# Performance work log

Measured on AMD Instinct MI355X. Metric: run time of the kernel, lower is better.

Reference implementation:

```python
import jax, jax.numpy as jnp
import numpy as np

DIM = 1024
HEADS = 16
HEAD_DIM = DIM // HEADS
SCALE = HEAD_DIM ** -0.5


def setup_inputs() -> dict:
    key = jax.random.key(0)
    k_x, k_win, k_wout, k_bout = jax.random.split(key, 4)
    x = jax.random.normal(k_x, (4, 2048, DIM), dtype=jnp.float32)
    # torch Linear: y = x @ W.T + b; store weights as [in, out] for jnp
    w_in = jax.random.normal(k_win, (DIM, 3 * DIM), dtype=jnp.float32) * (DIM ** -0.5)
    w_out = jax.random.normal(k_wout, (DIM, DIM), dtype=jnp.float32) * (DIM ** -0.5)
    b_out = jax.random.normal(k_bout, (DIM,), dtype=jnp.float32) * 0.02
    return {"x": x, "w_in": w_in, "w_out": w_out, "b_out": b_out}


def reference(x, w_in, w_out, b_out):
    b, n, _ = x.shape
    qkv = x @ w_in  # [b, n, 3*dim]
    q, k, v = jnp.split(qkv, 3, axis=-1)
    # [b, n, h*d] -> [b, h, n, d]
    def split_heads(t):
        return t.reshape(b, n, HEADS, HEAD_DIM).transpose(0, 2, 1, 3)
    q, k, v = split_heads(q), split_heads(k), split_heads(v)
    scores = jnp.einsum('bhid,bhjd->bhij', q, k) * SCALE
    attn = jax.nn.softmax(scores, axis=-1)  # dropout_rate=0 -> identity
    o = jnp.einsum('bhij,bhjd->bhid', attn, v)
    o = o.transpose(0, 2, 1, 3).reshape(b, n, HEADS * HEAD_DIM)
    return o @ w_out + b_out
```

## Files before the change

### kernel.cpp

```cpp
#include <hip/hip_runtime.h>

typedef unsigned short u16;
typedef __bf16 bf16x8 __attribute__((ext_vector_type(8)));
typedef float f32x4 __attribute__((ext_vector_type(4)));
typedef unsigned short u16x4 __attribute__((ext_vector_type(4)));
typedef unsigned short u16x8 __attribute__((ext_vector_type(8)));

#define DIM 1024
#define HEADS 16
#define HD 64
#define SEQ 2048
#define BATCH 4
#define NROWS (BATCH*SEQ)
#define C2 0.18033688f
#define THR_PS 1.125899907e15f

__device__ __forceinline__ u16 f2bf(float f) {
  union { float f; unsigned u; } v; v.f = f;
  unsigned r = v.u + 0x7FFFu + ((v.u >> 16) & 1u);
  return (u16)(r >> 16);
}

__device__ __forceinline__ unsigned cvt_pk_bf16(float lo, float hi) {
  unsigned r;
  asm("v_cvt_pk_bf16_f32 %0, %1, %2" : "=v"(r) : "v"(lo), "v"(hi));
  return r;
}

__device__ __forceinline__ f32x4 mfma16(bf16x8 a, bf16x8 b, f32x4 c) {
  return __builtin_amdgcn_mfma_f32_16x16x32_bf16(a, b, c, 0, 0, 0);
}

__device__ __forceinline__ void gl_lds16(const void* g, void* l) {
  __builtin_amdgcn_global_load_lds(
      (const __attribute__((address_space(1))) void*)g,
      (__attribute__((address_space(3))) void*)l, 16, 0, 0);
}

__global__ __launch_bounds__(256) void prep_kernel(const float* __restrict__ x,
                                                   const float* __restrict__ w_in,
                                                   const float* __restrict__ w_out,
                                                   u16* __restrict__ xb,
                                                   u16* __restrict__ w_inT,
                                                   u16* __restrict__ w_outT) {
  __shared__ u16 tile[64][65];
  const int bid = blockIdx.x;
  const int tid = threadIdx.x;
  if (bid < 8192) {
    int i = bid * 256 + tid;
    float4 v = ((const float4*)x)[i];
    u16x4 o = { f2bf(v.x), f2bf(v.y), f2bf(v.z), f2bf(v.w) };
    *(u16x4*)(xb + (size_t)i * 4) = o;
    return;
  }
  const float* in;
  u16* out;
  int R, C, c0, r0;
  if (bid < 8960) {
    int b2 = bid - 8192;
    in = w_in; out = w_inT; R = 1024; C = 3072;
    c0 = (b2 % 48) * 64; r0 = (b2 / 48) * 64;
  } else {
    int b3 = bid - 8960;
    in = w_out; out = w_outT; R = 1024; C = 1024;
    c0 = (b3 % 16) * 64; r0 = (b3 / 16) * 64;
  }
#pragma unroll
  for (int i = 0; i < 16; ++i) {
    int idx = tid + i * 256;
    int r = idx >> 6, c = idx & 63;
    tile[c][r] = f2bf(in[(size_t)(r0 + r) * C + c0 + c]);
  }
  __syncthreads();
#pragma unroll
  for (int i = 0; i < 16; ++i) {
    int idx = tid + i * 256;
    int r = idx >> 6, c = idx & 63;
    out[(size_t)(c0 + r) * R + r0 + c] = tile[r][c];
  }
}

__global__ __launch_bounds__(256) void transpose_v(const u16* __restrict__ qkv,
                                                   u16* __restrict__ vT) {
  __shared__ unsigned t32[64][37];
  const int t = blockIdx.x, bh = blockIdx.y;
  const int b = bh >> 4, h = bh & 15;
  const u16* src = qkv + ((size_t)(b * SEQ + t * 64)) * 3072 + 2048 + h * 64;
  const int tid = threadIdx.x;
#pragma unroll
  for (int i = 0; i < 8; ++i) {
    int lin = tid + i * 256;
    int r2 = lin >> 6, c = lin & 63;
    unsigned lo = src[(size_t)(2 * r2) * 3072 + c];
    unsigned hi = src[(size_t)(2 * r2 + 1) * 3072 + c];
    t32[c][r2] = lo | (hi << 16);
  }
  __syncthreads();
  unsigned* dst = (unsigned*)(vT + (size_t)bh * 64 * 2048);
#pragma unroll
  for (int i = 0; i < 8; ++i) {
    int lin = tid + i * 256;
    int d = lin >> 5, r2 = lin & 31;
    int rp = (r2 & 16) | ((r2 & 6) << 1) | ((r2 & 8) >> 2) | (r2 & 1);
    dst[(size_t)d * 1024 + t * 32 + rp] = t32[d][r2];
  }
}

template<int OUT_F32>
__global__ __launch_bounds__(256) void gemm_bt(const u16* __restrict__ A,
                                               const u16* __restrict__ BT,
                                               void* __restrict__ Cout,
                                               const float* __restrict__ bias,
                                               int M, int N, int K, int nx) {
  __shared__ __align__(16) u16 As[128 * 64];
  __shared__ __align__(16) u16 Bs[128 * 64];
  const int tid = threadIdx.x;
  const int l = tid & 63, w = tid >> 6, g = l >> 4, ln = l & 15;
  const int cpx = gridDim.x >> 3;
  const int jj = (blockIdx.x & 7) * cpx + (blockIdx.x >> 3);
  const int n0 = (jj % nx) * 128, m0 = (jj / nx) * 128;
  const int wr = w >> 1, wc = w & 1;
  f32x4 acc[4][4];
#pragma unroll
  for (int i = 0; i < 4; ++i)
#pragma unroll
    for (int j = 0; j < 4; ++j) acc[i][j] = (f32x4){0.f, 0.f, 0.f, 0.f};

  const int srow = tid >> 3;
  const int scol = (tid & 7) * 8;
  const u16* Asrc = A  + (size_t)(m0 + srow) * K + scol;
  const u16* Bsrc = BT + (size_t)(n0 + srow) * K + scol;
  char* AsB = (char*)As + (size_t)w * 1024;
  char* BsB = (char*)Bs + (size_t)w * 1024;

  const int nk = K >> 6;
  for (int kt = 0; kt < nk; ++kt) {
    const u16* a0 = Asrc + kt * 64;
    const u16* b0 = Bsrc + kt * 64;
#pragma unroll
    for (int is = 0; is < 4; ++is) {
      gl_lds16(a0 + (size_t)is * 32 * K, AsB + is * 4096);
      gl_lds16(b0 + (size_t)is * 32 * K, BsB + is * 4096);
    }
    __syncthreads();
#pragma unroll
    for (int kk = 0; kk < 2; ++kk) {
      bf16x8 af[4], bfr[4];
#pragma unroll
      for (int i = 0; i < 4; ++i) {
        af[i]  = *(const bf16x8*)(As + (wr * 64 + i * 16 + ln) * 64 + kk * 32 + g * 8);
        bfr[i] = *(const bf16x8*)(Bs + (wc * 64 + i * 16 + ln) * 64 + kk * 32 + g * 8);
      }
#pragma unroll
      for (int mi = 0; mi < 4; ++mi)
#pragma unroll
        for (int ni = 0; ni < 4; ++ni)
          acc[mi][ni] = mfma16(af[mi], bfr[ni], acc[mi][ni]);
    }
    __syncthreads();
  }
#pragma unroll
  for (int mi = 0; mi < 4; ++mi) {
#pragma unroll
    for (int ni = 0; ni < 4; ++ni) {
      int col = n0 + wc * 64 + ni * 16 + ln;
#pragma unroll
      for (int j = 0; j < 4; ++j) {
        int row = m0 + wr * 64 + mi * 16 + g * 4 + j;
        float v = acc[mi][ni][j];
        if (OUT_F32) {
          ((float*)Cout)[(size_t)row * N + col] = v + bias[col];
        } else {
          ((u16*)Cout)[(size_t)row * N + col] = f2bf(v);
        }
      }
    }
  }
}

__global__ __launch_bounds__(256) void attn_kernel(const u16* __restrict__ qkv,
                                                   const u16* __restrict__ vT,
                                                   u16* __restrict__ obuf) {
  __shared__ __align__(16) u16 k_lds[2][64 * 64];
  __shared__ __align__(16) u16 v_lds[2][64 * 64];
  const int wg = blockIdx.x;
  const int j = (wg & 7) * 128 + (wg >> 3);
  const int qt = j & 15, h = (j >> 4) & 15, b = j >> 8;
  const int tid = threadIdx.x;
  const int w = tid >> 6, l = tid & 63, g = l >> 4, ln = l & 15;
  const int qbase = qt * 128 + w * 32;
  const size_t rs = 3 * DIM;

  bf16x8 qf[2][2];
#pragma unroll
  for (int e = 0; e < 2; ++e) {
    const u16* qb = qkv + (size_t)(b * SEQ + qbase + e * 16 + ln) * rs + h * HD;
    qf[e][0] = *(const bf16x8*)(qb + g * 8);
    qf[e][1] = *(const bf16x8*)(qb + 32 + g * 8);
  }

  const int krow = tid >> 3;
  const int ksrccol = ((((tid & 7) << 4) ^ ((krow & 7) << 4))) >> 1;
  const u16* kbase = qkv + (size_t)b * SEQ * rs + DIM + h * HD;
  const u16* vtb = vT + (size_t)(b * HEADS + h) * 64 * 2048;
  const int swz = (ln & 7) << 4;

  float m[2] = { -1e30f, -1e30f }, psac[2] = { 0.f, 0.f };
  f32x4 of[2][4];
#pragma unroll
  for (int e = 0; e < 2; ++e)
#pragma unroll
    for (int i = 0; i < 4; ++i) of[e][i] = (f32x4){0.f, 0.f, 0.f, 0.f};

  auto stage = [&](int buf, int kv0) {
    const u16* ks0 = kbase + (size_t)(kv0 + krow) * rs + ksrccol;
    const u16* vs0 = vtb + (size_t)krow * 2048 + kv0 + ksrccol;
    char* kd = (char*)(&k_lds[buf][0]) + (size_t)w * 1024;
    char* vd = (char*)(&v_lds[buf][0]) + (size_t)w * 1024;
    gl_lds16(ks0, kd);
    gl_lds16(ks0 + (size_t)32 * rs, kd + 4096);
    gl_lds16(vs0, vd);
    gl_lds16(vs0 + (size_t)32 * 2048, vd + 4096);
  };

  stage(0, 0);
  __syncthreads();
  int cur = 0;

  for (int t = 0; t < 32; ++t) {
    if (t < 31) stage(cur ^ 1, (t + 1) * 64);

    f32x4 sacc[2][4];
#pragma unroll
    for (int e = 0; e < 2; ++e)
#pragma unroll
      for (int f = 0; f < 4; ++f) sacc[e][f] = (f32x4){0.f, 0.f, 0.f, 0.f};
    __builtin_amdgcn_s_setprio(1);
#pragma unroll
    for (int f = 0; f < 4; ++f) {
      const char* kr = (const char*)(&k_lds[cur][0]) + (f * 16 + ln) * 128;
      bf16x8 a0 = *(const bf16x8*)(kr + ((g * 16) ^ swz));
      bf16x8 a1 = *(const bf16x8*)(kr + ((64 | (g * 16)) ^ swz));
#pragma unroll
      for (int e = 0; e < 2; ++e) {
        sacc[e][f] = mfma16(a0, qf[e][0], sacc[e][f]);
        sacc[e][f] = mfma16(a1, qf[e][1], sacc[e][f]);
      }
    }
    __builtin_amdgcn_s_setprio(0);

    union pu { unsigned wd[4]; bf16x8 bv; } pf[2][2];
    float ps[2];
#pragma unroll
    for (int e = 0; e < 2; ++e) {
      const float mc = m[e] * C2;
      float s2 = 0.f;
#pragma unroll
      for (int f = 0; f < 4; ++f)
#pragma unroll
        for (int j2 = 0; j2 < 2; ++j2) {
          float p0 = __builtin_amdgcn_exp2f(fmaf(sacc[e][f][2 * j2], C2, -mc));
          float p1 = __builtin_amdgcn_exp2f(fmaf(sacc[e][f][2 * j2 + 1], C2, -mc));
          s2 += p0 + p1;
          pf[e][f >> 1].wd[(f & 1) * 2 + j2] = cvt_pk_bf16(p0, p1);
        }
      ps[e] = s2;
    }
    if (__any(fmaxf(ps[0], ps[1]) > THR_PS)) {
#pragma unroll
      for (int e = 0; e < 2; ++e) {
        float tm = -3e38f;
#pragma unroll
        for (int f = 0; f < 4; ++f)
#pragma unroll
          for (int jj = 0; jj < 4; ++jj) tm = fmaxf(tm, sacc[e][f][jj]);
        tm = fmaxf(tm, __shfl_xor(tm, 16));
        tm = fmaxf(tm, __shfl_xor(tm, 32));
        float mn = fmaxf(m[e], tm);
        float rc = __builtin_amdgcn_exp2f((m[e] - mn) * C2);
        psac[e] *= rc;
#pragma unroll
        for (int fd = 0; fd < 4; ++fd) of[e][fd] *= rc;
        m[e] = mn;
        const float mc = mn * C2;
        float s2 = 0.f;
#pragma unroll
        for (int f = 0; f < 4; ++f)
#pragma unroll
          for (int j2 = 0; j2 < 2; ++j2) {
            float p0 = __builtin_amdgcn_exp2f(fmaf(sacc[e][f][2 * j2], C2, -mc));
            float p1 = __builtin_amdgcn_exp2f(fmaf(sacc[e][f][2 * j2 + 1], C2, -mc));
            s2 += p0 + p1;
            pf[e][f >> 1].wd[(f & 1) * 2 + j2] = cvt_pk_bf16(p0, p1);
          }
        ps[e] = s2;
      }
    }
    psac[0] += ps[0];
    psac[1] += ps[1];

    __builtin_amdgcn_s_setprio(1);
#pragma unroll
    for (int kk = 0; kk < 2; ++kk)
#pragma unroll
      for (int fd = 0; fd < 4; ++fd) {
        const char* vr = (const char*)(&v_lds[cur][0]) + (fd * 16 + ln) * 128;
        bf16x8 fa = *(const bf16x8*)(vr + ((kk * 64 + g * 16) ^ swz));
#pragma unroll
        for (int e = 0; e < 2; ++e)
          of[e][fd] = mfma16(fa, pf[e][kk].bv, of[e][fd]);
      }
    __builtin_amdgcn_s_setprio(0);

    __syncthreads();
    cur ^= 1;
  }

#pragma unroll
  for (int e = 0; e < 2; ++e) {
    float ls = psac[e];
    ls += __shfl_xor(ls, 16);
    ls += __shfl_xor(ls, 32);
    float linv = 1.f / ls;
    u16* orow = obuf + (size_t)(b * SEQ + qbase + e * 16 + ln) * DIM + h * HD;
#pragma unroll
    for (int fd = 0; fd < 4; ++fd) {
      unsigned w0 = cvt_pk_bf16(of[e][fd][0] * linv, of[e][fd][1] * linv);
      unsigned w1 = cvt_pk_bf16(of[e][fd][2] * linv, of[e][fd][3] * linv);
      unsigned* dst = (unsigned*)(orow + fd * 16 + g * 4);
      dst[0] = w0;
      dst[1] = w1;
    }
  }
}

extern "C" void kernel_launch(void* const* d_in, const int* in_sizes, int n_in,
                              void* d_out, int out_size, void* d_ws, size_t ws_size,
                              hipStream_t stream) {
  const float* x     = (const float*)d_in[0];
  const float* w_in  = (const float*)d_in[1];
  const float* w_out = (const float*)d_in[2];
  const float* b_out = (const float*)d_in[3];
  float* out = (float*)d_out;

  char* ws = (char*)d_ws;
  u16* xb     = (u16*)(ws);
  u16* vT     = (u16*)(ws);
  u16* w_inT  = (u16*)(ws + (size_t)16 * 1024 * 1024);
  u16* w_outT = (u16*)(ws + (size_t)22 * 1024 * 1024);
  u16* qkv    = (u16*)(ws + (size_t)24 * 1024 * 1024);
  u16* obuf   = (u16*)(ws + (size_t)72 * 1024 * 1024);

  prep_kernel<<<9216, 256, 0, stream>>>(x, w_in, w_out, xb, w_inT, w_outT);
  gemm_bt<0><<<1536, 256, 0, stream>>>(xb, w_inT, qkv, nullptr, NROWS, 3 * DIM, DIM, 24);
  transpose_v<<<dim3(32, 64), 256, 0, stream>>>(qkv, vT);
  attn_kernel<<<1024, 256, 0, stream>>>(qkv, vT, obuf);
  gemm_bt<1><<<512, 256, 0, stream>>>(obuf, w_outT, out, b_out, NROWS, DIM, DIM, 8);
}
```

Baseline: 231.9 us.

## Shrink attention workgroups to two waves and drop K/V double buffering

The attention kernel now runs 128-thread workgroups that each cover 64 query rows, launching twice as many blocks. The K/V LDS staging goes from a double-buffered prefetch to a single buffer loaded at the top of each iteration and followed by a barrier. This halves LDS per block and raises the number of resident workgroups per CU, relying on other workgroups to hide load latency in place of in-block prefetch. Each K/V tile is now loaded by half as many query rows, which doubles global/L2 traffic for K and V, and the load stalls are exposed inside each block.

```diff
diff --git a/kernel.cpp b/kernel.cpp
--- a/kernel.cpp
+++ b/kernel.cpp
@@ -178,17 +178,17 @@
   }
 }
 
-__global__ __launch_bounds__(256) void attn_kernel(const u16* __restrict__ qkv,
+__global__ __launch_bounds__(128) void attn_kernel(const u16* __restrict__ qkv,
                                                    const u16* __restrict__ vT,
                                                    u16* __restrict__ obuf) {
-  __shared__ __align__(16) u16 k_lds[2][64 * 64];
-  __shared__ __align__(16) u16 v_lds[2][64 * 64];
+  __shared__ __align__(16) u16 k_lds[64 * 64];
+  __shared__ __align__(16) u16 v_lds[64 * 64];
   const int wg = blockIdx.x;
-  const int j = (wg & 7) * 128 + (wg >> 3);
-  const int qt = j & 15, h = (j >> 4) & 15, b = j >> 8;
+  const int j = (wg & 7) * 256 + (wg >> 3);
+  const int qt = j & 31, h = (j >> 5) & 15, b = j >> 9;
   const int tid = threadIdx.x;
   const int w = tid >> 6, l = tid & 63, g = l >> 4, ln = l & 15;
-  const int qbase = qt * 128 + w * 32;
+  const int qbase = qt * 64 + w * 32;
   const size_t rs = 3 * DIM;
 
   bf16x8 qf[2][2];
@@ -199,8 +199,9 @@
     qf[e][1] = *(const bf16x8*)(qb + 32 + g * 8);
   }
 
-  const int krow = tid >> 3;
-  const int ksrccol = ((((tid & 7) << 4) ^ ((krow & 7) << 4))) >> 1;
+  const int krlo = l >> 3;
+  const int scol = (((l & 7) ^ krlo) << 3);
+  const int rbase = w * 8 + krlo;
   const u16* kbase = qkv + (size_t)b * SEQ * rs + DIM + h * HD;
   const u16* vtb = vT + (size_t)(b * HEADS + h) * 64 * 2048;
   const int swz = (ln & 7) << 4;
@@ -212,23 +213,16 @@
 #pragma unroll
     for (int i = 0; i < 4; ++i) of[e][i] = (f32x4){0.f, 0.f, 0.f, 0.f};
 
-  auto stage = [&](int buf, int kv0) {
-    const u16* ks0 = kbase + (size_t)(kv0 + krow) * rs + ksrccol;
-    const u16* vs0 = vtb + (size_t)krow * 2048 + kv0 + ksrccol;
-    char* kd = (char*)(&k_lds[buf][0]) + (size_t)w * 1024;
-    char* vd = (char*)(&v_lds[buf][0]) + (size_t)w * 1024;
-    gl_lds16(ks0, kd);
-    gl_lds16(ks0 + (size_t)32 * rs, kd + 4096);
-    gl_lds16(vs0, vd);
-    gl_lds16(vs0 + (size_t)32 * 2048, vd + 4096);
-  };
-
-  stage(0, 0);
-  __syncthreads();
-  int cur = 0;
-
   for (int t = 0; t < 32; ++t) {
-    if (t < 31) stage(cur ^ 1, (t + 1) * 64);
+    const int kv0 = t * 64;
+    char* kd = (char*)k_lds + (size_t)w * 1024;
+    char* vd = (char*)v_lds + (size_t)w * 1024;
+#pragma unroll
+    for (int i = 0; i < 4; ++i) {
+      gl_lds16(kbase + (size_t)(kv0 + i * 16 + rbase) * rs + scol, kd + i * 2048);
+      gl_lds16(vtb + (size_t)(i * 16 + rbase) * 2048 + kv0 + scol, vd + i * 2048);
+    }
+    __syncthreads();
 
     f32x4 sacc[2][4];
 #pragma unroll
@@ -238,7 +232,7 @@
     __builtin_amdgcn_s_setprio(1);
 #pragma unroll
     for (int f = 0; f < 4; ++f) {
-      const char* kr = (const char*)(&k_lds[cur][0]) + (f * 16 + ln) * 128;
+      const char* kr = (const char*)k_lds + (f * 16 + ln) * 128;
       bf16x8 a0 = *(const bf16x8*)(kr + ((g * 16) ^ swz));
       bf16x8 a1 = *(const bf16x8*)(kr + ((64 | (g * 16)) ^ swz));
 #pragma unroll
@@ -304,7 +298,7 @@
     for (int kk = 0; kk < 2; ++kk)
 #pragma unroll
       for (int fd = 0; fd < 4; ++fd) {
-        const char* vr = (const char*)(&v_lds[cur][0]) + (fd * 16 + ln) * 128;
+        const char* vr = (const char*)v_lds + (fd * 16 + ln) * 128;
         bf16x8 fa = *(const bf16x8*)(vr + ((kk * 64 + g * 16) ^ swz));
 #pragma unroll
         for (int e = 0; e < 2; ++e)
@@ -313,7 +307,6 @@
     __builtin_amdgcn_s_setprio(0);
 
     __syncthreads();
-    cur ^= 1;
   }
 
 #pragma unroll
@@ -354,6 +347,6 @@
   prep_kernel<<<9216, 256, 0, stream>>>(x, w_in, w_out, xb, w_inT, w_outT);
   gemm_bt<0><<<1536, 256, 0, stream>>>(xb, w_inT, qkv, nullptr, NROWS, 3 * DIM, DIM, 24);
   transpose_v<<<dim3(32, 64), 256, 0, stream>>>(qkv, vT);
-  attn_kernel<<<1024, 256, 0, stream>>>(qkv, vT, obuf);
+  attn_kernel<<<2048, 128, 0, stream>>>(qkv, vT, obuf);
   gemm_bt<1><<<512, 256, 0, stream>>>(obuf, w_outT, out, b_out, NROWS, DIM, DIM, 8);
 }
```

Result: slower. 241.6 us (+4.2%).
